# Optimization experiments

Hardware: AMD Instinct MI355X
Metric: run time of the kernel (lower is better)

The kernel has to match this reference:

```python
import jax, jax.numpy as jnp
import numpy as np

N = 50000   # nodes
E = 800000  # edges (avg degree 16)
DIMS = [(128, 128), (128, 128), (128, 64)]  # (in, out) per SAGEConv layer
EPS_BN = 1e-5
EPS_NORM = 1e-12


def _make_layer(key, din, dout):
    k1, k2 = jax.random.split(key)
    s = 1.0 / np.sqrt(din)
    return (
        jax.random.normal(k1, (dout, din), jnp.float32) * s,  # Wl: neighbor linear
        jnp.zeros((dout,), jnp.float32),                      # bl
        jax.random.normal(k2, (dout, din), jnp.float32) * s,  # Wr: root linear (no bias in PyG)
        jnp.ones((dout,), jnp.float32),                       # bn gamma
        jnp.zeros((dout,), jnp.float32),                      # bn beta
        jnp.zeros((dout,), jnp.float32),                      # bn running mean
        jnp.ones((dout,), jnp.float32),                       # bn running var
    )


def setup_inputs() -> dict:
    key = jax.random.key(0)
    kx, ke, k0, k1, k2 = jax.random.split(key, 5)
    inp = {
        "x": jax.random.normal(kx, (N, 128), jnp.float32),
        "edge_index": jax.random.randint(ke, (2, E), 0, N, dtype=jnp.int32),
    }
    for i, (k, (din, dout)) in enumerate(zip([k0, k1, k2], DIMS)):
        Wl, bl, Wr, g, b, rm, rv = _make_layer(k, din, dout)
        inp.update({f"Wl{i}": Wl, f"bl{i}": bl, f"Wr{i}": Wr,
                    f"g{i}": g, f"b{i}": b, f"rm{i}": rm, f"rv{i}": rv})
    return inp


def _sage_conv(x, src, dst, Wl, bl, Wr):
    # mean aggregation of incoming messages: gather src features, scatter-add at dst
    agg = jax.ops.segment_sum(x[src], dst, num_segments=N)          # [N, din]
    deg = jax.ops.segment_sum(jnp.ones((src.shape[0],), x.dtype), dst, num_segments=N)
    mean = agg / jnp.maximum(deg, 1.0)[:, None]
    return mean @ Wl.T + bl + x @ Wr.T


def _bn_eval(x, g, b, rm, rv):
    return g * (x - rm) * jax.lax.rsqrt(rv + EPS_BN) + b


def reference(x, edge_index,
              Wl0, bl0, Wr0, g0, b0, rm0, rv0,
              Wl1, bl1, Wr1, g1, b1, rm1, rv1,
              Wl2, bl2, Wr2, g2, b2, rm2, rv2):
    src, dst = edge_index[0], edge_index[1]
    layers = [
        (Wl0, bl0, Wr0, g0, b0, rm0, rv0),
        (Wl1, bl1, Wr1, g1, b1, rm1, rv1),
        (Wl2, bl2, Wr2, g2, b2, rm2, rv2),
    ]
    h = x
    for i, (Wl, bl, Wr, g, b, rm, rv) in enumerate(layers):
        h = _bn_eval(_sage_conv(h, src, dst, Wl, bl, Wr), g, b, rm, rv)
        if i < len(layers) - 1:
            h = jax.nn.relu(h)  # dropout is identity in eval mode
    # F.normalize(p=2, dim=1)
    return h / jnp.maximum(jnp.linalg.norm(h, axis=1, keepdims=True), EPS_NORM)
```

## Files before the change

### kernel.cpp

```cpp
#include <hip/hip_runtime.h>
#include <hip/hip_bf16.h>

#define CDIV(a,b) (((a)+(b)-1)/(b))
#define NBUCK_MAX 512
#define FUSE_CAP 4096
#define AGGF_CAP 3072

typedef __attribute__((ext_vector_type(8))) short short8;
typedef __attribute__((ext_vector_type(4))) float f32x4;
typedef __attribute__((ext_vector_type(2))) float f32x2;

static __device__ __forceinline__ unsigned short f2bf(float f){
  union { float f; unsigned u; } v; v.f = f;
  unsigned r = v.u + 0x7fffu + ((v.u >> 16) & 1u);
  return (unsigned short)(r >> 16);
}
static __device__ __forceinline__ unsigned pack2(float lo, float hi){
  return (unsigned)f2bf(lo) | ((unsigned)f2bf(hi) << 16);
}
static __device__ __forceinline__ float bf2f(unsigned short s){
  union { unsigned u; float f; } v; v.u = ((unsigned)s) << 16; return v.f;
}
static __device__ __forceinline__ unsigned pk_fp8x4(float a, float b, float c, float d){
  int v = __builtin_amdgcn_cvt_pk_fp8_f32(a, b, 0, false);
  v = __builtin_amdgcn_cvt_pk_fp8_f32(c, d, v, true);
  return (unsigned)v;
}

#define ACCP16(v) { b0 += __builtin_amdgcn_cvt_pk_f32_fp8((int)v.x, false); \
                    b1 += __builtin_amdgcn_cvt_pk_f32_fp8((int)v.x, true);  \
                    b2 += __builtin_amdgcn_cvt_pk_f32_fp8((int)v.y, false); \
                    b3 += __builtin_amdgcn_cvt_pk_f32_fp8((int)v.y, true);  \
                    b4 += __builtin_amdgcn_cvt_pk_f32_fp8((int)v.z, false); \
                    b5 += __builtin_amdgcn_cvt_pk_f32_fp8((int)v.z, true);  \
                    b6 += __builtin_amdgcn_cvt_pk_f32_fp8((int)v.w, false); \
                    b7 += __builtin_amdgcn_cvt_pk_f32_fp8((int)v.w, true); }


struct WtpArgs {
  const float *W0, *W1, *bl, *g, *b, *rm, *rv;
  unsigned short* Bpk; float *sc; float *sh;
  int kblk, dout, do_bn, nblk, perm;
};

static __device__ __forceinline__ void wtp_one(const WtpArgs& a, int idx){
  int NB16 = a.kblk*32*a.dout;
  if (idx < NB16){
    int j = idx & 7, lane = (idx >> 3) & 63, rest = idx >> 9;
    int NT = a.dout >> 4;
    int nt = rest % NT, kk = rest / NT;
    int nn = nt*16 + (lane & 15);
    int k  = kk*32 + ((lane >> 4) * 8) + j;
    float v;
    if (k < 128){
      int kc = a.perm ? (((k & 7) << 4) | (k >> 3)) : k;
      v = a.W0[nn*128 + kc];
    } else {
      v = a.W1[nn*128 + (k - 128)];
    }
    a.Bpk[idx] = f2bf(v);
  } else if (a.do_bn && idx < NB16 + a.dout){
    int jj = idx - NB16;
    float s = a.g[jj] * rsqrtf(a.rv[jj] + 1e-5f);
    a.sc[jj] = s;
    a.sh[jj] = (a.bl[jj] - a.rm[jj]) * s + a.b[jj];
  }
}


__global__ __launch_bounds__(256) void k_prep(const float* __restrict__ x, int n4, unsigned* __restrict__ xb,
                                              unsigned* __restrict__ xq,
                                              const int* __restrict__ dst, int E,
                                              int* __restrict__ bcnt, int nbuck,
                                              int castBlocks, int histBlocks,
                                              WtpArgs a0, WtpArgs a1, WtpArgs a2, WtpArgs a3){
  __shared__ int s[NBUCK_MAX];
  int b = blockIdx.x, t = threadIdx.x;
  if (b < castBlocks){
    int i = b*256 + t;
    if (i < n4){
      float4 v = ((const float4*)x)[i];
      uint2 o; o.x = pack2(v.x, v.y); o.y = pack2(v.z, v.w);
      ((uint2*)xb)[i] = o;
      xq[i] = pk_fp8x4(v.x, v.y, v.z, v.w);
    }
    return;
  }
  b -= castBlocks;
  if (b < histBlocks){
    for (int i=t;i<nbuck;i+=256) s[i] = 0;
    __syncthreads();
    constexpr int EPT = 16;
    int e0 = b*256*EPT;
    #pragma unroll
    for (int i=0;i<EPT;i++){
      int e = e0 + i*256 + t;
      if (e < E) atomicAdd(&s[dst[e] >> 7], 1);
    }
    __syncthreads();
    for (int i=t;i<nbuck;i+=256){
      int c = s[i];
      if (c > 0) atomicAdd(&bcnt[i], c);
    }
    return;
  }
  b -= histBlocks;
  if (b < a0.nblk){ wtp_one(a0, b*256 + t); return; }
  b -= a0.nblk;
  if (b < a1.nblk){ wtp_one(a1, b*256 + t); return; }
  b -= a1.nblk;
  if (b < a2.nblk){ wtp_one(a2, b*256 + t); return; }
  b -= a2.nblk;
  wtp_one(a3, b*256 + t);
}

__global__ __launch_bounds__(256) void k_bucketA(const int* __restrict__ src, const int* __restrict__ dst,
                                                 int E, const int* __restrict__ bcnt,
                                                 int* __restrict__ bcur, unsigned* __restrict__ ebuf, int nbuck){
  __shared__ int scnt[NBUCK_MAX];
  __shared__ int sbase[NBUCK_MAX];
  __shared__ int sboff[NBUCK_MAX];
  __shared__ int ss[256];
  int t = threadIdx.x;
  {
    int a0 = (2*t   < nbuck) ? bcnt[2*t]   : 0;
    int a1 = (2*t+1 < nbuck) ? bcnt[2*t+1] : 0;
    ss[t] = a0 + a1; __syncthreads();
    for (int d=1; d<256; d<<=1){
      int u = (t>=d) ? ss[t-d] : 0;
      __syncthreads();
      ss[t] += u;
      __syncthreads();
    }
    int excl = ss[t] - (a0 + a1);
    if (2*t   < nbuck) sboff[2*t]   = excl;
    if (2*t+1 < nbuck) sboff[2*t+1] = excl + a0;
  }
  for (int i=t;i<nbuck;i+=256) scnt[i] = 0;
  __syncthreads();
  constexpr int EPT = 16;
  int e0 = blockIdx.x*256*EPT;
  int b[EPT]; unsigned pk[EPT];
  #pragma unroll
  for (int i=0;i<EPT;i++){
    int e = e0 + i*256 + t;
    if (e < E){
      int d = dst[e];
      b[i] = d >> 7;
      pk[i] = ((unsigned)(d & 127) << 16) | (unsigned)src[e];
      atomicAdd(&scnt[b[i]], 1);
    } else b[i] = -1;
  }
  __syncthreads();
  for (int i=t;i<nbuck;i+=256){
    int c = scnt[i];
    sbase[i] = (c > 0) ? atomicAdd(&bcur[i], c) : 0;
    scnt[i] = 0;
  }
  __syncthreads();
  #pragma unroll
  for (int i=0;i<EPT;i++){
    if (b[i] >= 0){
      int p = atomicAdd(&scnt[b[i]], 1);
      ebuf[(size_t)sboff[b[i]] + sbase[b[i]] + p] = pk[i];
    }
  }
}

__global__ __launch_bounds__(256) void k_bucketB(const unsigned* __restrict__ ebuf, const int* __restrict__ bcnt,
                                                 int nbuck, int E, int N,
                                                 int* __restrict__ offR, int* __restrict__ csr,
                                                 int* __restrict__ nodemap){
  __shared__ int sEx[NBUCK_MAX];
  __shared__ int ss[256];
  __shared__ int sdeg[128];
  __shared__ int sabs[129];
  __shared__ int cur[128];
  __shared__ unsigned skey[128];
  __shared__ int rof[128];
  int b = blockIdx.x, t = threadIdx.x;
  {
    int a0 = (2*t   < nbuck) ? bcnt[2*t]   : 0;
    int a1 = (2*t+1 < nbuck) ? bcnt[2*t+1] : 0;
    ss[t] = a0 + a1; __syncthreads();
    for (int d=1; d<256; d<<=1){
      int u = (t>=d) ? ss[t-d] : 0;
      __syncthreads();
      ss[t] += u;
      __syncthreads();
    }
    int excl = ss[t] - (a0 + a1);
    if (2*t   < nbuck) sEx[2*t]   = excl;
    if (2*t+1 < nbuck) sEx[2*t+1] = excl + a0;
  }
  if (t < 128){ sdeg[t] = 0; cur[t] = 0; }
  __syncthreads();
  int e0 = sEx[b];
  int e1 = (b+1 < nbuck) ? sEx[b+1] : E;
  for (int e = e0 + t; e < e1; e += 256)
    atomicAdd(&sdeg[ebuf[e] >> 16], 1);
  __syncthreads();
  if (t < 128) skey[t] = ((unsigned)sdeg[t] << 7) | (unsigned)(127 - t);
  __syncthreads();
  #pragma unroll
  for (int k=2; k<=128; k<<=1){
    #pragma unroll
    for (int j=k>>1; j>0; j>>=1){
      if (t < 128){
        int p = t ^ j;
        if (p > t){
          unsigned x = skey[t], y = skey[p];
          bool swap = ((t & k) == 0) ? (x < y) : (x > y);
          if (swap){ skey[t] = y; skey[p] = x; }
        }
      }
      __syncthreads();
    }
  }
  if (t < 128){
    int lid = 127 - (int)(skey[t] & 127u);
    rof[lid] = t;
    sdeg[t] = (int)(skey[t] >> 7);
  }
  __syncthreads();
  for (int d=1; d<128; d<<=1){
    int u = (t < 128 && t >= d) ? sdeg[t-d] : 0;
    __syncthreads();
    if (t < 128) sdeg[t] += u;
    __syncthreads();
  }
  if (t == 0) sabs[0] = e0;
  if (t < 128) sabs[t+1] = e0 + sdeg[t];
  __syncthreads();
  int n0 = b << 7, n1 = min(n0 + 128, N);
  int cnt = n1 - n0;
  if (t <= cnt) offR[n0 + t] = sabs[t];
  if (t < cnt)  nodemap[n0 + t] = n0 + (127 - (int)(skey[t] & 127u));
  for (int e = e0 + t; e < e1; e += 256){
    unsigned pr = ebuf[e];
    int ln = (int)(pr >> 16);
    int p = atomicAdd(&cur[ln], 1);
    csr[sabs[rof[ln]] + p] = (int)(pr & 0xffffu);
  }
}


template<bool YL>
__global__ __launch_bounds__(256, 2) void k_fuse(
    const uint4* __restrict__ hq4, const int* __restrict__ offR, const int* __restrict__ csr,
    const int* __restrict__ nodemap,
    const unsigned short* __restrict__ Ag, const unsigned short* __restrict__ Bpk,
    const float* __restrict__ sc, const float* __restrict__ sh,
    const unsigned short* __restrict__ BpkL,
    unsigned short* __restrict__ outh, unsigned* __restrict__ outq,
    unsigned* __restrict__ outyl, int n){
  __shared__ uint4 Ms4[128*17];
  __shared__ uint4 sBL4[1024];
  __shared__ int sw[2];
  unsigned short* Ms = (unsigned short*)Ms4;
  int* scsr = (int*)sBL4;
  int t = threadIdx.x;
  int mb = blockIdx.x*128;
  if (t < 2) sw[t] = offR[min(mb + t*128, n)];
  __syncthreads();
  int e0b = sw[0];
  int span = sw[1] - e0b;
  for (int i = t; i < span && i < FUSE_CAP; i += 256) scsr[i] = csr[e0b + i];
  __syncthreads();

  int lane = t & 63, w = t >> 6;
  int sl = lane & 7;

  #pragma unroll
  for (int it=0; it<4; it++){
    int rk = w*32 + it*8 + (lane >> 3);
    int idx = mb + rk;
    bool valid = idx < n;
    int s0 = valid ? offR[idx]   : 0;
    int s1 = valid ? offR[idx+1] : 0;
    int ln = valid ? (nodemap[idx] - mb) : rk;
    f32x2 b0={0,0},b1={0,0},b2={0,0},b3={0,0},b4={0,0},b5={0,0},b6={0,0},b7={0,0};
    int e = s0;
    for (; e + 8 <= s1; e += 8){
      int le = e - e0b;
      int i0,i1,i2,i3,i4,i5,i6,i7;
      if (le + 8 <= FUSE_CAP){
        i0 = scsr[le];   i1 = scsr[le+1]; i2 = scsr[le+2]; i3 = scsr[le+3];
        i4 = scsr[le+4]; i5 = scsr[le+5]; i6 = scsr[le+6]; i7 = scsr[le+7];
      } else {
        i0 = csr[e];   i1 = csr[e+1]; i2 = csr[e+2]; i3 = csr[e+3];
        i4 = csr[e+4]; i5 = csr[e+5]; i6 = csr[e+6]; i7 = csr[e+7];
      }
      uint4 v0 = hq4[(size_t)i0*8 + sl];
      uint4 v1 = hq4[(size_t)i1*8 + sl];
      uint4 v2 = hq4[(size_t)i2*8 + sl];
      uint4 v3 = hq4[(size_t)i3*8 + sl];
      uint4 v4 = hq4[(size_t)i4*8 + sl];
      uint4 v5 = hq4[(size_t)i5*8 + sl];
      uint4 v6 = hq4[(size_t)i6*8 + sl];
      uint4 v7 = hq4[(size_t)i7*8 + sl];
      ACCP16(v0); ACCP16(v1); ACCP16(v2); ACCP16(v3);
      ACCP16(v4); ACCP16(v5); ACCP16(v6); ACCP16(v7);
    }
    for (; e + 4 <= s1; e += 4){
      int le = e - e0b;
      int i0,i1,i2,i3;
      if (le + 4 <= FUSE_CAP){
        i0 = scsr[le]; i1 = scsr[le+1]; i2 = scsr[le+2]; i3 = scsr[le+3];
      } else {
        i0 = csr[e]; i1 = csr[e+1]; i2 = csr[e+2]; i3 = csr[e+3];
      }
      uint4 v0 = hq4[(size_t)i0*8 + sl];
      uint4 v1 = hq4[(size_t)i1*8 + sl];
      uint4 v2 = hq4[(size_t)i2*8 + sl];
      uint4 v3 = hq4[(size_t)i3*8 + sl];
      ACCP16(v0); ACCP16(v1); ACCP16(v2); ACCP16(v3);
    }
    for (; e < s1; e++){
      int le = e - e0b;
      int ii = (le < FUSE_CAP) ? scsr[le] : csr[e];
      uint4 v = hq4[(size_t)ii*8 + sl];
      ACCP16(v);
    }
    int d = s1 - s0;
    float inv = 1.0f / (float)(d > 0 ? d : 1);
    uint4 o0, o1;
    o0.x = pack2(b0.x*inv, b0.y*inv);  o0.y = pack2(b1.x*inv, b1.y*inv);
    o0.z = pack2(b2.x*inv, b2.y*inv);  o0.w = pack2(b3.x*inv, b3.y*inv);
    o1.x = pack2(b4.x*inv, b4.y*inv);  o1.y = pack2(b5.x*inv, b5.y*inv);
    o1.z = pack2(b6.x*inv, b6.y*inv);  o1.w = pack2(b7.x*inv, b7.y*inv);
    Ms4[ln*17 + sl*2]     = o0;
    Ms4[ln*17 + sl*2 + 1] = o1;
  }
  __syncthreads();

  int quad = lane >> 4, c = lane & 15;
  int woff = w*32;
  int r0 = mb + woff + c;
  int r1 = r0 + 16;

  f32x4 acc[2][8];
  #pragma unroll
  for (int mt=0;mt<2;mt++)
    #pragma unroll
    for (int nt=0;nt<8;nt++) acc[mt][nt] = (f32x4){0.f,0.f,0.f,0.f};

  #pragma unroll
  for (int kk=0; kk<8; kk++){
    int ka = (kk & 3)*32 + quad*8;
    short8 a0, a1;
    if (kk < 4){
      a0 = *(const short8*)&Ms[(woff + c)*136 + ka];
      a1 = *(const short8*)&Ms[(woff + c + 16)*136 + ka];
    } else {
      a0 = (short8){0,0,0,0,0,0,0,0}; a1 = (short8){0,0,0,0,0,0,0,0};
      if (r0 < n) a0 = *(const short8*)(Ag + (size_t)r0*128 + ka);
      if (r1 < n) a1 = *(const short8*)(Ag + (size_t)r1*128 + ka);
    }
    #pragma unroll
    for (int nt=0; nt<8; nt++){
      short8 b = *(const short8*)(Bpk + (size_t)((kk*8 + nt)*64 + lane)*8);
      acc[0][nt] = __builtin_amdgcn_mfma_f32_16x16x32_bf16(a0, b, acc[0][nt], 0, 0, 0);
      acc[1][nt] = __builtin_amdgcn_mfma_f32_16x16x32_bf16(a1, b, acc[1][nt], 0, 0, 0);
    }
  }

  float scv[8], shv[8];
  #pragma unroll
  for (int nt=0;nt<8;nt++){ scv[nt] = sc[nt*16 + c]; shv[nt] = sh[nt*16 + c]; }

  if constexpr (YL) __syncthreads();

  #pragma unroll
  for (int mt=0; mt<2; mt++){
    #pragma unroll
    for (int r=0;r<4;r++){
      int lrow = woff + mt*16 + quad*4 + r;
      int row = mb + lrow;
      if (row < n){
        float u[8];
        #pragma unroll
        for (int nt=0;nt<8;nt++){
          float uu = acc[mt][nt][r]*scv[nt] + shv[nt];
          u[nt] = fmaxf(uu, 0.f);
          outh[(size_t)row*128 + nt*16 + c] = f2bf(u[nt]);
        }
        if constexpr (!YL){
          uint2 q;
          q.x = pk_fp8x4(u[0], u[1], u[2], u[3]);
          q.y = pk_fp8x4(u[4], u[5], u[6], u[7]);
          ((uint2*)outq)[(size_t)row*16 + c] = q;
        } else {
          #pragma unroll
          for (int nt=0;nt<8;nt++) Ms[lrow*136 + nt*16 + c] = f2bf(u[nt]);
        }
      } else if constexpr (YL) {
        #pragma unroll
        for (int nt=0;nt<8;nt++) Ms[lrow*136 + nt*16 + c] = 0;
      }
    }
  }

  if constexpr (YL){
    {
      const uint4* sL = (const uint4*)BpkL;
      #pragma unroll
      for (int i=0;i<4;i++) sBL4[i*256 + t] = sL[i*256 + t];
    }
    __syncthreads();
    unsigned short* BsL = (unsigned short*)sBL4;
    f32x4 acc2[2][4];
    #pragma unroll
    for (int mt=0;mt<2;mt++)
      #pragma unroll
      for (int nt=0;nt<4;nt++) acc2[mt][nt] = (f32x4){0.f,0.f,0.f,0.f};
    int r0l = woff + c, r1l = r0l + 16;
    #pragma unroll
    for (int kk=0; kk<4; kk++){
      int ka = kk*32 + quad*8;
      short8 a0 = *(const short8*)&Ms[r0l*136 + ka];
      short8 a1 = *(const short8*)&Ms[r1l*136 + ka];
      #pragma unroll
      for (int nt=0; nt<4; nt++){
        short8 b = *(const short8*)&BsL[(size_t)((kk*4 + nt)*64 + lane)*8];
        acc2[0][nt] = __builtin_amdgcn_mfma_f32_16x16x32_bf16(a0, b, acc2[0][nt], 0, 0, 0);
        acc2[1][nt] = __builtin_amdgcn_mfma_f32_16x16x32_bf16(a1, b, acc2[1][nt], 0, 0, 0);
      }
    }
    #pragma unroll
    for (int mt=0; mt<2; mt++){
      #pragma unroll
      for (int r=0;r<4;r++){
        int row = mb + woff + mt*16 + quad*4 + r;
        if (row < n){
          unsigned q  = pk_fp8x4(acc2[0][0][r], acc2[0][1][r], acc2[0][2][r], acc2[0][3][r]);
          unsigned q1 = pk_fp8x4(acc2[1][0][r], acc2[1][1][r], acc2[1][2][r], acc2[1][3][r]);
          outyl[(size_t)row*16 + c] = (mt == 0) ? q : q1;
        }
      }
    }
  }
}


__global__ __launch_bounds__(256, 2) void k_aggf(
    const uint4* __restrict__ ylq4, const int* __restrict__ offR, const int* __restrict__ csr,
    const int* __restrict__ nodemap,
    const unsigned short* __restrict__ A0, const unsigned short* __restrict__ BpkR,
    const float* __restrict__ sc, const float* __restrict__ sh,
    float* __restrict__ outf, int n){
  __shared__ unsigned short Ms[128*64];
  __shared__ unsigned short Bs[128*64];
  __shared__ int scsr[AGGF_CAP];
  __shared__ int sw[2];
  int t = threadIdx.x;
  int mb = blockIdx.x*128;
  if (t < 2) sw[t] = offR[min(mb + t*128, n)];
  {
    const uint4* s = (const uint4*)BpkR;
    uint4* d = (uint4*)Bs;
    #pragma unroll
    for (int i=0;i<4;i++) d[i*256 + t] = s[i*256 + t];
  }
  __syncthreads();
  int e0b = sw[0];
  int span = sw[1] - e0b;
  for (int i = t; i < span && i < AGGF_CAP; i += 256) scsr[i] = csr[e0b + i];
  __syncthreads();

  int lane = t & 63, w = t >> 6;
  int sl4 = lane & 3;

  #pragma unroll
  for (int it=0; it<2; it++){
    int rk = w*32 + it*16 + (lane >> 2);
    int idx = mb + rk;
    bool valid = idx < n;
    int s0 = valid ? offR[idx]   : 0;
    int s1 = valid ? offR[idx+1] : 0;
    int ln = valid ? (nodemap[idx] - mb) : rk;
    f32x2 b0={0,0},b1={0,0},b2={0,0},b3={0,0},b4={0,0},b5={0,0},b6={0,0},b7={0,0};
    int e = s0;
    for (; e + 8 <= s1; e += 8){
      int le = e - e0b;
      int i0,i1,i2,i3,i4,i5,i6,i7;
      if (le + 8 <= AGGF_CAP){
        i0 = scsr[le];   i1 = scsr[le+1]; i2 = scsr[le+2]; i3 = scsr[le+3];
        i4 = scsr[le+4]; i5 = scsr[le+5]; i6 = scsr[le+6]; i7 = scsr[le+7];
      } else {
        i0 = csr[e];   i1 = csr[e+1]; i2 = csr[e+2]; i3 = csr[e+3];
        i4 = csr[e+4]; i5 = csr[e+5]; i6 = csr[e+6]; i7 = csr[e+7];
      }
      uint4 v0 = ylq4[(size_t)i0*4 + sl4];
      uint4 v1 = ylq4[(size_t)i1*4 + sl4];
      uint4 v2 = ylq4[(size_t)i2*4 + sl4];
      uint4 v3 = ylq4[(size_t)i3*4 + sl4];
      uint4 v4 = ylq4[(size_t)i4*4 + sl4];
      uint4 v5 = ylq4[(size_t)i5*4 + sl4];
      uint4 v6 = ylq4[(size_t)i6*4 + sl4];
      uint4 v7 = ylq4[(size_t)i7*4 + sl4];
      ACCP16(v0); ACCP16(v1); ACCP16(v2); ACCP16(v3);
      ACCP16(v4); ACCP16(v5); ACCP16(v6); ACCP16(v7);
    }
    for (; e + 4 <= s1; e += 4){
      int le = e - e0b;
      int i0,i1,i2,i3;
      if (le + 4 <= AGGF_CAP){
        i0 = scsr[le]; i1 = scsr[le+1]; i2 = scsr[le+2]; i3 = scsr[le+3];
      } else {
        i0 = csr[e]; i1 = csr[e+1]; i2 = csr[e+2]; i3 = csr[e+3];
      }
      uint4 v0 = ylq4[(size_t)i0*4 + sl4];
      uint4 v1 = ylq4[(size_t)i1*4 + sl4];
      uint4 v2 = ylq4[(size_t)i2*4 + sl4];
      uint4 v3 = ylq4[(size_t)i3*4 + sl4];
      ACCP16(v0); ACCP16(v1); ACCP16(v2); ACCP16(v3);
    }
    for (; e < s1; e++){
      int le = e - e0b;
      int ii = (le < AGGF_CAP) ? scsr[le] : csr[e];
      uint4 v = ylq4[(size_t)ii*4 + sl4];
      ACCP16(v);
    }
    int d = s1 - s0;
    float inv = 1.0f / (float)(d > 0 ? d : 1);
    uint4 o0, o1;
    o0.x = pack2(b0.x*inv, b0.y*inv);  o0.y = pack2(b1.x*inv, b1.y*inv);
    o0.z = pack2(b2.x*inv, b2.y*inv);  o0.w = pack2(b3.x*inv, b3.y*inv);
    o1.x = pack2(b4.x*inv, b4.y*inv);  o1.y = pack2(b5.x*inv, b5.y*inv);
    o1.z = pack2(b6.x*inv, b6.y*inv);  o1.w = pack2(b7.x*inv, b7.y*inv);
    ((uint4*)Ms)[ln*8 + sl4*2]     = o0;
    ((uint4*)Ms)[ln*8 + sl4*2 + 1] = o1;
  }
  __syncthreads();

  int quad = lane >> 4, c = lane & 15;
  int woff = w*32;
  int r0 = mb + woff + c;
  int r1 = r0 + 16;
  f32x4 acc[2][4];
  #pragma unroll
  for (int mt=0;mt<2;mt++)
    #pragma unroll
    for (int nt=0;nt<4;nt++) acc[mt][nt] = (f32x4){0.f,0.f,0.f,0.f};
  #pragma unroll
  for (int kk=0; kk<4; kk++){
    int ka = kk*32 + quad*8;
    short8 a0 = {0,0,0,0,0,0,0,0}, a1 = {0,0,0,0,0,0,0,0};
    if (r0 < n) a0 = *(const short8*)(A0 + (size_t)r0*128 + ka);
    if (r1 < n) a1 = *(const short8*)(A0 + (size_t)r1*128 + ka);
    #pragma unroll
    for (int nt=0; nt<4; nt++){
      short8 b = *(const short8*)&Bs[(size_t)((kk*4 + nt)*64 + lane)*8];
      acc[0][nt] = __builtin_amdgcn_mfma_f32_16x16x32_bf16(a0, b, acc[0][nt], 0, 0, 0);
      acc[1][nt] = __builtin_amdgcn_mfma_f32_16x16x32_bf16(a1, b, acc[1][nt], 0, 0, 0);
    }
  }

  float scv[4], shv[4];
  #pragma unroll
  for (int nt=0;nt<4;nt++){ scv[nt] = sc[nt*16 + c]; shv[nt] = sh[nt*16 + c]; }

  #pragma unroll
  for (int mt=0; mt<2; mt++){
    #pragma unroll
    for (int r=0;r<4;r++){
      int lr = woff + mt*16 + quad*4 + r;
      int row = mb + lr;
      float v[4];
      float ss = 0.f;
      if (row < n){
        #pragma unroll
        for (int nt=0;nt<4;nt++){
          float u = acc[mt][nt][r] + bf2f(Ms[lr*64 + c*4 + nt]);
          u = u*scv[nt] + shv[nt];
          v[nt] = u;
          ss += u*u;
        }
      } else {
        #pragma unroll
        for (int nt=0;nt<4;nt++) v[nt] = 0.f;
      }
      ss += __shfl_xor(ss, 1, 64);
      ss += __shfl_xor(ss, 2, 64);
      ss += __shfl_xor(ss, 4, 64);
      ss += __shfl_xor(ss, 8, 64);
      float rn = 1.0f / fmaxf(sqrtf(ss), 1e-12f);
      if (row < n){
        #pragma unroll
        for (int nt=0;nt<4;nt++) outf[(size_t)row*64 + nt*16 + c] = v[nt]*rn;
      }
    }
  }
}


extern "C" void kernel_launch(void* const* d_in, const int* in_sizes, int n_in,
                              void* d_out, int out_size, void* d_ws, size_t ws_size,
                              hipStream_t stream){
  const float* x = (const float*)d_in[0];
  const int* ei  = (const int*)d_in[1];
  int N = in_sizes[0] / 128;
  int E = in_sizes[1] / 2;
  const int* esrc = ei;
  const int* edst = ei + E;
  int nbuck = CDIV(N, 128);

  const float *Wl[3], *bl[3], *Wr[3], *g[3], *bb[3], *rm[3], *rv[3];
  int dout[3];
  for (int i=0;i<3;i++){
    int base = 2 + 7*i;
    Wl[i]=(const float*)d_in[base];   bl[i]=(const float*)d_in[base+1];
    Wr[i]=(const float*)d_in[base+2]; g[i] =(const float*)d_in[base+3];
    bb[i]=(const float*)d_in[base+4]; rm[i]=(const float*)d_in[base+5];
    rv[i]=(const float*)d_in[base+6];
    dout[i] = in_sizes[base] / 128;
  }

  char* p = (char*)d_ws;
  size_t o = 0;
  auto alloc = [&](size_t bytes)->void*{ void* r = p + o; o += (bytes + 255) & ~(size_t)255; return r; };
  int* bz    = (int*)alloc((size_t)2*nbuck*4);
  int* bcnt  = bz;
  int* bcur  = bz + nbuck;
  int* offR  = (int*)alloc((size_t)(N+1)*4);
  int* nodemap = (int*)alloc((size_t)N*4);
  int* csr   = (int*)alloc((size_t)E*4);
  unsigned* ebuf = (unsigned*)alloc((size_t)E*4);
  unsigned* xb   = (unsigned*)alloc((size_t)N*64*4);
  unsigned* xq   = (unsigned*)alloc((size_t)N*128);
  unsigned* h_a  = (unsigned*)alloc((size_t)N*64*4);
  unsigned* haq  = (unsigned*)alloc((size_t)N*128);
  unsigned* h_b  = (unsigned*)alloc((size_t)N*64*4);
  unsigned* ylb  = (unsigned*)alloc((size_t)N*64);
  unsigned short* Bpk01[2];
  float* sc[3]; float* sh[3];
  for (int i=0;i<2;i++) Bpk01[i] = (unsigned short*)alloc((size_t)256*dout[i]*2);
  unsigned short* BpkL = (unsigned short*)alloc((size_t)128*dout[2]*2);
  unsigned short* BpkR = (unsigned short*)alloc((size_t)128*dout[2]*2);
  for (int i=0;i<3;i++){
    sc[i] = (float*)alloc((size_t)dout[i]*4);
    sh[i] = (float*)alloc((size_t)dout[i]*4);
  }

  hipMemsetAsync(bz, 0, (size_t)2*nbuck*4, stream);

  WtpArgs wa[4];
  wa[0] = { Wl[0], Wr[0], bl[0], g[0], bb[0], rm[0], rv[0], Bpk01[0], sc[0], sh[0], 8, dout[0], 1, CDIV(256*dout[0]+dout[0],256), 0 };
  wa[1] = { Wl[1], Wr[1], bl[1], g[1], bb[1], rm[1], rv[1], Bpk01[1], sc[1], sh[1], 8, dout[1], 1, CDIV(256*dout[1]+dout[1],256), 1 };
  wa[2] = { Wl[2], nullptr, nullptr, nullptr, nullptr, nullptr, nullptr, BpkL, nullptr, nullptr, 4, dout[2], 0, CDIV(128*dout[2],256), 0 };
  wa[3] = { Wr[2], nullptr, bl[2], g[2], bb[2], rm[2], rv[2], BpkR, sc[2], sh[2], 4, dout[2], 1, CDIV(128*dout[2]+dout[2],256), 0 };

  int castBlocks = CDIV(N*32, 256);
  int histBlocks = CDIV(E, 256*16);
  int prepBlocks = castBlocks + histBlocks + wa[0].nblk + wa[1].nblk + wa[2].nblk + wa[3].nblk;
  k_prep   <<<prepBlocks,256,0,stream>>>(x, N*32, xb, xq, edst, E, bcnt, nbuck, castBlocks, histBlocks,
                                         wa[0], wa[1], wa[2], wa[3]);
  k_bucketA<<<CDIV(E,256*16),256,0,stream>>>(esrc, edst, E, bcnt, bcur, ebuf, nbuck);
  k_bucketB<<<nbuck,256,0,stream>>>(ebuf, bcnt, nbuck, E, N, offR, csr, nodemap);

  k_fuse<false><<<nbuck,256,0,stream>>>((const uint4*)xq, offR, csr, nodemap,
                                        (const unsigned short*)xb, Bpk01[0], sc[0], sh[0], nullptr,
                                        (unsigned short*)h_a, haq, nullptr, N);
  k_fuse<true><<<nbuck,256,0,stream>>>((const uint4*)haq, offR, csr, nodemap,
                                       (const unsigned short*)h_a, Bpk01[1], sc[1], sh[1], BpkL,
                                       (unsigned short*)h_b, nullptr, ylb, N);
  k_aggf<<<nbuck,256,0,stream>>>((const uint4*)ylb, offR, csr, nodemap,
                                 (const unsigned short*)h_b, BpkR, sc[2], sh[2],
                                 (float*)d_out, N);
}
```

Baseline: 242.8 us.

## Fuse CSR bucket build into first SAGE layer and drop degree-sorted node remap

Merges the second bucketing pass (per-bucket CSR construction) with the first layer's gather-aggregate-GEMM kernel, building the bucket's CSR slice directly in shared memory and reusing it for aggregation. The bitonic sort of nodes by degree and the nodemap indirection are removed, so rows are processed in natural order. Launch bounds are raised to allow three blocks per CU. This removes one kernel launch, a global CSR round-trip, and the sort barriers, at the cost of losing degree-based load balancing within waves and extra shared memory in the fused kernel.

```diff
diff --git a/kernel.cpp b/kernel.cpp
--- a/kernel.cpp
+++ b/kernel.cpp
@@ -3,8 +3,7 @@
 
 #define CDIV(a,b) (((a)+(b)-1)/(b))
 #define NBUCK_MAX 512
-#define FUSE_CAP 4096
-#define AGGF_CAP 3072
+#define FUSE_CAP 3072
 
 typedef __attribute__((ext_vector_type(8))) short short8;
 typedef __attribute__((ext_vector_type(4))) float f32x4;
@@ -167,17 +166,21 @@
   }
 }
 
-__global__ __launch_bounds__(256) void k_bucketB(const unsigned* __restrict__ ebuf, const int* __restrict__ bcnt,
-                                                 int nbuck, int E, int N,
-                                                 int* __restrict__ offR, int* __restrict__ csr,
-                                                 int* __restrict__ nodemap){
+
+__global__ __launch_bounds__(256, 3) void k_bfuse(
+    const unsigned* __restrict__ ebuf, const int* __restrict__ bcnt, int nbuck, int E, int N,
+    int* __restrict__ off, int* __restrict__ csr,
+    const uint4* __restrict__ xq4, const unsigned short* __restrict__ Ag,
+    const unsigned short* __restrict__ Bpk, const float* __restrict__ sc, const float* __restrict__ sh,
+    unsigned short* __restrict__ outh, unsigned* __restrict__ outq){
+  __shared__ uint4 Ms4[128*17];
+  __shared__ int scsr[FUSE_CAP];
   __shared__ int sEx[NBUCK_MAX];
   __shared__ int ss[256];
-  __shared__ int sdeg[128];
-  __shared__ int sabs[129];
-  __shared__ int cur[128];
-  __shared__ unsigned skey[128];
-  __shared__ int rof[128];
+  unsigned short* Ms = (unsigned short*)Ms4;
+  int* sdeg = (int*)Ms4;
+  int* sabs = sdeg + 128;
+  int* cur  = sabs + 129;
   int b = blockIdx.x, t = threadIdx.x;
   {
     int a0 = (2*t   < nbuck) ? bcnt[2*t]   : 0;
@@ -197,31 +200,10 @@
   __syncthreads();
   int e0 = sEx[b];
   int e1 = (b+1 < nbuck) ? sEx[b+1] : E;
+  int span = e1 - e0;
+  bool fits = span <= FUSE_CAP;
   for (int e = e0 + t; e < e1; e += 256)
     atomicAdd(&sdeg[ebuf[e] >> 16], 1);
-  __syncthreads();
-  if (t < 128) skey[t] = ((unsigned)sdeg[t] << 7) | (unsigned)(127 - t);
-  __syncthreads();
-  #pragma unroll
-  for (int k=2; k<=128; k<<=1){
-    #pragma unroll
-    for (int j=k>>1; j>0; j>>=1){
-      if (t < 128){
-        int p = t ^ j;
-        if (p > t){
-          unsigned x = skey[t], y = skey[p];
-          bool swap = ((t & k) == 0) ? (x < y) : (x > y);
-          if (swap){ skey[t] = y; skey[p] = x; }
-        }
-      }
-      __syncthreads();
-    }
-  }
-  if (t < 128){
-    int lid = 127 - (int)(skey[t] & 127u);
-    rof[lid] = t;
-    sdeg[t] = (int)(skey[t] >> 7);
-  }
   __syncthreads();
   for (int d=1; d<128; d<<=1){
     int u = (t < 128 && t >= d) ? sdeg[t-d] : 0;
@@ -229,31 +211,157 @@
     if (t < 128) sdeg[t] += u;
     __syncthreads();
   }
-  if (t == 0) sabs[0] = e0;
-  if (t < 128) sabs[t+1] = e0 + sdeg[t];
+  if (t == 0) sabs[0] = 0;
+  if (t < 128) sabs[t+1] = sdeg[t];
   __syncthreads();
   int n0 = b << 7, n1 = min(n0 + 128, N);
   int cnt = n1 - n0;
-  if (t <= cnt) offR[n0 + t] = sabs[t];
-  if (t < cnt)  nodemap[n0 + t] = n0 + (127 - (int)(skey[t] & 127u));
+  if (t <= cnt) off[n0 + t] = e0 + sabs[t];
+  int lane = t & 63, w = t >> 6, sl = lane & 7;
+  int gs0[4], gs1[4];
+  #pragma unroll
+  for (int it=0; it<4; it++){
+    int rk = w*32 + it*8 + (lane >> 3);
+    gs0[it] = sabs[rk];
+    gs1[it] = sabs[rk+1];
+  }
   for (int e = e0 + t; e < e1; e += 256){
     unsigned pr = ebuf[e];
     int ln = (int)(pr >> 16);
     int p = atomicAdd(&cur[ln], 1);
-    csr[sabs[rof[ln]] + p] = (int)(pr & 0xffffu);
-  }
-}
-
-
-template<bool YL>
-__global__ __launch_bounds__(256, 2) void k_fuse(
-    const uint4* __restrict__ hq4, const int* __restrict__ offR, const int* __restrict__ csr,
-    const int* __restrict__ nodemap,
+    int loc = sabs[ln] + p;
+    int sv = (int)(pr & 0xffffu);
+    if (fits) scsr[loc] = sv;
+    else      csr[e0 + loc] = sv;
+  }
+  __syncthreads();
+  if (fits){
+    for (int i = t; i < span; i += 256) csr[e0 + i] = scsr[i];
+  } else {
+    for (int i = t; i < FUSE_CAP; i += 256) scsr[i] = csr[e0 + i];
+    __syncthreads();
+  }
+
+  #pragma unroll
+  for (int it=0; it<4; it++){
+    int rk = w*32 + it*8 + (lane >> 3);
+    int s0 = gs0[it], s1 = gs1[it];
+    f32x2 b0={0,0},b1={0,0},b2={0,0},b3={0,0},b4={0,0},b5={0,0},b6={0,0},b7={0,0};
+    int e = s0;
+    for (; e + 8 <= s1; e += 8){
+      int i0,i1,i2,i3,i4,i5,i6,i7;
+      if (e + 8 <= FUSE_CAP){
+        i0 = scsr[e];   i1 = scsr[e+1]; i2 = scsr[e+2]; i3 = scsr[e+3];
+        i4 = scsr[e+4]; i5 = scsr[e+5]; i6 = scsr[e+6]; i7 = scsr[e+7];
+      } else {
+        i0 = csr[e0+e];   i1 = csr[e0+e+1]; i2 = csr[e0+e+2]; i3 = csr[e0+e+3];
+        i4 = csr[e0+e+4]; i5 = csr[e0+e+5]; i6 = csr[e0+e+6]; i7 = csr[e0+e+7];
+      }
+      uint4 v0 = xq4[(size_t)i0*8 + sl];
+      uint4 v1 = xq4[(size_t)i1*8 + sl];
+      uint4 v2 = xq4[(size_t)i2*8 + sl];
+      uint4 v3 = xq4[(size_t)i3*8 + sl];
+      uint4 v4 = xq4[(size_t)i4*8 + sl];
+      uint4 v5 = xq4[(size_t)i5*8 + sl];
+      uint4 v6 = xq4[(size_t)i6*8 + sl];
+      uint4 v7 = xq4[(size_t)i7*8 + sl];
+      ACCP16(v0); ACCP16(v1); ACCP16(v2); ACCP16(v3);
+      ACCP16(v4); ACCP16(v5); ACCP16(v6); ACCP16(v7);
+    }
+    for (; e + 4 <= s1; e += 4){
+      int i0,i1,i2,i3;
+      if (e + 4 <= FUSE_CAP){
+        i0 = scsr[e]; i1 = scsr[e+1]; i2 = scsr[e+2]; i3 = scsr[e+3];
+      } else {
+        i0 = csr[e0+e]; i1 = csr[e0+e+1]; i2 = csr[e0+e+2]; i3 = csr[e0+e+3];
+      }
+      uint4 v0 = xq4[(size_t)i0*8 + sl];
+      uint4 v1 = xq4[(size_t)i1*8 + sl];
+      uint4 v2 = xq4[(size_t)i2*8 + sl];
+      uint4 v3 = xq4[(size_t)i3*8 + sl];
+      ACCP16(v0); ACCP16(v1); ACCP16(v2); ACCP16(v3);
+    }
+    for (; e < s1; e++){
+      int ii = (e < FUSE_CAP) ? scsr[e] : csr[e0+e];
+      uint4 v = xq4[(size_t)ii*8 + sl];
+      ACCP16(v);
+    }
+    int d = s1 - s0;
+    float inv = 1.0f / (float)(d > 0 ? d : 1);
+    uint4 o0, o1;
+    o0.x = pack2(b0.x*inv, b0.y*inv);  o0.y = pack2(b1.x*inv, b1.y*inv);
+    o0.z = pack2(b2.x*inv, b2.y*inv);  o0.w = pack2(b3.x*inv, b3.y*inv);
+    o1.x = pack2(b4.x*inv, b4.y*inv);  o1.y = pack2(b5.x*inv, b5.y*inv);
+    o1.z = pack2(b6.x*inv, b6.y*inv);  o1.w = pack2(b7.x*inv, b7.y*inv);
+    Ms4[rk*17 + sl*2]     = o0;
+    Ms4[rk*17 + sl*2 + 1] = o1;
+  }
+  __syncthreads();
+
+  int quad = lane >> 4, c = lane & 15;
+  int mb = n0, woff = w*32;
+  int r0 = mb + woff + c;
+  int r1 = r0 + 16;
+
+  f32x4 acc[2][8];
+  #pragma unroll
+  for (int mt=0;mt<2;mt++)
+    #pragma unroll
+    for (int nt=0;nt<8;nt++) acc[mt][nt] = (f32x4){0.f,0.f,0.f,0.f};
+
+  #pragma unroll
+  for (int kk=0; kk<8; kk++){
+    int ka = (kk & 3)*32 + quad*8;
+    short8 a0, a1;
+    if (kk < 4){
+      a0 = *(const short8*)&Ms[(woff + c)*136 + ka];
+      a1 = *(const short8*)&Ms[(woff + c + 16)*136 + ka];
+    } else {
+      a0 = (short8){0,0,0,0,0,0,0,0}; a1 = (short8){0,0,0,0,0,0,0,0};
+      if (r0 < N) a0 = *(const short8*)(Ag + (size_t)r0*128 + ka);
+      if (r1 < N) a1 = *(const short8*)(Ag + (size_t)r1*128 + ka);
+    }
+    #pragma unroll
+    for (int nt=0; nt<8; nt++){
+      short8 bb = *(const short8*)(Bpk + (size_t)((kk*8 + nt)*64 + lane)*8);
+      acc[0][nt] = __builtin_amdgcn_mfma_f32_16x16x32_bf16(a0, bb, acc[0][nt], 0, 0, 0);
+      acc[1][nt] = __builtin_amdgcn_mfma_f32_16x16x32_bf16(a1, bb, acc[1][nt], 0, 0, 0);
+    }
+  }
+
+  float scv[8], shv[8];
+  #pragma unroll
+  for (int nt=0;nt<8;nt++){ scv[nt] = sc[nt*16 + c]; shv[nt] = sh[nt*16 + c]; }
+
+  #pragma unroll
+  for (int mt=0; mt<2; mt++){
+    #pragma unroll
+    for (int r=0;r<4;r++){
+      int row = mb + woff + mt*16 + quad*4 + r;
+      if (row < N){
+        float u[8];
+        #pragma unroll
+        for (int nt=0;nt<8;nt++){
+          float uu = acc[mt][nt][r]*scv[nt] + shv[nt];
+          u[nt] = fmaxf(uu, 0.f);
+          outh[(size_t)row*128 + nt*16 + c] = f2bf(u[nt]);
+        }
+        uint2 q;
+        q.x = pk_fp8x4(u[0], u[1], u[2], u[3]);
+        q.y = pk_fp8x4(u[4], u[5], u[6], u[7]);
+        ((uint2*)outq)[(size_t)row*16 + c] = q;
+      }
+    }
+  }
+}
+
+
+__global__ __launch_bounds__(256, 3) void k_fuse1(
+    const uint4* __restrict__ hq4, const int* __restrict__ off, const int* __restrict__ csr,
     const unsigned short* __restrict__ Ag, const unsigned short* __restrict__ Bpk,
     const float* __restrict__ sc, const float* __restrict__ sh,
     const unsigned short* __restrict__ BpkL,
-    unsigned short* __restrict__ outh, unsigned* __restrict__ outq,
-    unsigned* __restrict__ outyl, int n){
+    unsigned short* __restrict__ outh, unsigned* __restrict__ outyl, int n){
   __shared__ uint4 Ms4[128*17];
   __shared__ uint4 sBL4[1024];
   __shared__ int sw[2];
@@ -261,11 +369,12 @@
   int* scsr = (int*)sBL4;
   int t = threadIdx.x;
   int mb = blockIdx.x*128;
-  if (t < 2) sw[t] = offR[min(mb + t*128, n)];
+  if (t < 2) sw[t] = off[min(mb + t*128, n)];
   __syncthreads();
   int e0b = sw[0];
   int span = sw[1] - e0b;
-  for (int i = t; i < span && i < FUSE_CAP; i += 256) scsr[i] = csr[e0b + i];
+  int CAPL = 4096;
+  for (int i = t; i < span && i < CAPL; i += 256) scsr[i] = csr[e0b + i];
   __syncthreads();
 
   int lane = t & 63, w = t >> 6;
@@ -276,15 +385,14 @@
     int rk = w*32 + it*8 + (lane >> 3);
     int idx = mb + rk;
     bool valid = idx < n;
-    int s0 = valid ? offR[idx]   : 0;
-    int s1 = valid ? offR[idx+1] : 0;
-    int ln = valid ? (nodemap[idx] - mb) : rk;
+    int s0 = valid ? off[idx]   : 0;
+    int s1 = valid ? off[idx+1] : 0;
     f32x2 b0={0,0},b1={0,0},b2={0,0},b3={0,0},b4={0,0},b5={0,0},b6={0,0},b7={0,0};
     int e = s0;
     for (; e + 8 <= s1; e += 8){
       int le = e - e0b;
       int i0,i1,i2,i3,i4,i5,i6,i7;
-      if (le + 8 <= FUSE_CAP){
+      if (le + 8 <= CAPL){
         i0 = scsr[le];   i1 = scsr[le+1]; i2 = scsr[le+2]; i3 = scsr[le+3];
         i4 = scsr[le+4]; i5 = scsr[le+5]; i6 = scsr[le+6]; i7 = scsr[le+7];
       } else {
@@ -305,7 +413,7 @@
     for (; e + 4 <= s1; e += 4){
       int le = e - e0b;
       int i0,i1,i2,i3;
-      if (le + 4 <= FUSE_CAP){
+      if (le + 4 <= CAPL){
         i0 = scsr[le]; i1 = scsr[le+1]; i2 = scsr[le+2]; i3 = scsr[le+3];
       } else {
         i0 = csr[e]; i1 = csr[e+1]; i2 = csr[e+2]; i3 = csr[e+3];
@@ -318,7 +426,7 @@
     }
     for (; e < s1; e++){
       int le = e - e0b;
-      int ii = (le < FUSE_CAP) ? scsr[le] : csr[e];
+      int ii = (le < CAPL) ? scsr[le] : csr[e];
       uint4 v = hq4[(size_t)ii*8 + sl];
       ACCP16(v);
     }
@@ -329,8 +437,8 @@
     o0.z = pack2(b2.x*inv, b2.y*inv);  o0.w = pack2(b3.x*inv, b3.y*inv);
     o1.x = pack2(b4.x*inv, b4.y*inv);  o1.y = pack2(b5.x*inv, b5.y*inv);
     o1.z = pack2(b6.x*inv, b6.y*inv);  o1.w = pack2(b7.x*inv, b7.y*inv);
-    Ms4[ln*17 + sl*2]     = o0;
-    Ms4[ln*17 + sl*2 + 1] = o1;
+    Ms4[rk*17 + sl*2]     = o0;
+    Ms4[rk*17 + sl*2 + 1] = o1;
   }
   __syncthreads();
 
@@ -359,9 +467,9 @@
     }
     #pragma unroll
     for (int nt=0; nt<8; nt++){
-      short8 b = *(const short8*)(Bpk + (size_t)((kk*8 + nt)*64 + lane)*8);
-      acc[0][nt] = __builtin_amdgcn_mfma_f32_16x16x32_bf16(a0, b, acc[0][nt], 0, 0, 0);
-      acc[1][nt] = __builtin_amdgcn_mfma_f32_16x16x32_bf16(a1, b, acc[1][nt], 0, 0, 0);
+      short8 bb = *(const short8*)(Bpk + (size_t)((kk*8 + nt)*64 + lane)*8);
+      acc[0][nt] = __builtin_amdgcn_mfma_f32_16x16x32_bf16(a0, bb, acc[0][nt], 0, 0, 0);
+      acc[1][nt] = __builtin_amdgcn_mfma_f32_16x16x32_bf16(a1, bb, acc[1][nt], 0, 0, 0);
     }
   }
 
@@ -369,7 +477,7 @@
   #pragma unroll
   for (int nt=0;nt<8;nt++){ scv[nt] = sc[nt*16 + c]; shv[nt] = sh[nt*16 + c]; }
 
-  if constexpr (YL) __syncthreads();
+  __syncthreads();
 
   #pragma unroll
   for (int mt=0; mt<2; mt++){
@@ -385,67 +493,59 @@
           u[nt] = fmaxf(uu, 0.f);
           outh[(size_t)row*128 + nt*16 + c] = f2bf(u[nt]);
         }
-        if constexpr (!YL){
-          uint2 q;
-          q.x = pk_fp8x4(u[0], u[1], u[2], u[3]);
-          q.y = pk_fp8x4(u[4], u[5], u[6], u[7]);
-          ((uint2*)outq)[(size_t)row*16 + c] = q;
-        } else {
-          #pragma unroll
-          for (int nt=0;nt<8;nt++) Ms[lrow*136 + nt*16 + c] = f2bf(u[nt]);
-        }
-      } else if constexpr (YL) {
+        #pragma unroll
+        for (int nt=0;nt<8;nt++) Ms[lrow*136 + nt*16 + c] = f2bf(u[nt]);
+      } else {
         #pragma unroll
         for (int nt=0;nt<8;nt++) Ms[lrow*136 + nt*16 + c] = 0;
       }
     }
   }
 
-  if constexpr (YL){
-    {
-      const uint4* sL = (const uint4*)BpkL;
-      #pragma unroll
-      for (int i=0;i<4;i++) sBL4[i*256 + t] = sL[i*256 + t];
-    }
-    __syncthreads();
-    unsigned short* BsL = (unsigned short*)sBL4;
-    f32x4 acc2[2][4];
-    #pragma unroll
-    for (int mt=0;mt<2;mt++)
-      #pragma unroll
-      for (int nt=0;nt<4;nt++) acc2[mt][nt] = (f32x4){0.f,0.f,0.f,0.f};
-    int r0l = woff + c, r1l = r0l + 16;
-    #pragma unroll
-    for (int kk=0; kk<4; kk++){
-      int ka = kk*32 + quad*8;
-      short8 a0 = *(const short8*)&Ms[r0l*136 + ka];
-      short8 a1 = *(const short8*)&Ms[r1l*136 + ka];
-      #pragma unroll
-      for (int nt=0; nt<4; nt++){
-        short8 b = *(const short8*)&BsL[(size_t)((kk*4 + nt)*64 + lane)*8];
-        acc2[0][nt] = __builtin_amdgcn_mfma_f32_16x16x32_bf16(a0, b, acc2[0][nt], 0, 0, 0);
-        acc2[1][nt] = __builtin_amdgcn_mfma_f32_16x16x32_bf16(a1, b, acc2[1][nt], 0, 0, 0);
-      }
-    }
-    #pragma unroll
-    for (int mt=0; mt<2; mt++){
-      #pragma unroll
-      for (int r=0;r<4;r++){
-        int row = mb + woff + mt*16 + quad*4 + r;
-        if (row < n){
-          unsigned q  = pk_fp8x4(acc2[0][0][r], acc2[0][1][r], acc2[0][2][r], acc2[0][3][r]);
-          unsigned q1 = pk_fp8x4(acc2[1][0][r], acc2[1][1][r], acc2[1][2][r], acc2[1][3][r]);
-          outyl[(size_t)row*16 + c] = (mt == 0) ? q : q1;
-        }
-      }
-    }
-  }
-}
-
-
-__global__ __launch_bounds__(256, 2) void k_aggf(
-    const uint4* __restrict__ ylq4, const int* __restrict__ offR, const int* __restrict__ csr,
-    const int* __restrict__ nodemap,
+  {
+    const uint4* sL = (const uint4*)BpkL;
+    #pragma unroll
+    for (int i=0;i<4;i++) sBL4[i*256 + t] = sL[i*256 + t];
+  }
+  __syncthreads();
+  unsigned short* BsL = (unsigned short*)sBL4;
+  f32x4 acc2[2][4];
+  #pragma unroll
+  for (int mt=0;mt<2;mt++)
+    #pragma unroll
+    for (int nt=0;nt<4;nt++) acc2[mt][nt] = (f32x4){0.f,0.f,0.f,0.f};
+  int r0l = woff + c, r1l = r0l + 16;
+  #pragma unroll
+  for (int kk=0; kk<4; kk++){
+    int ka = kk*32 + quad*8;
+    short8 a0 = *(const short8*)&Ms[r0l*136 + ka];
+    short8 a1 = *(const short8*)&Ms[r1l*136 + ka];
+    #pragma unroll
+    for (int nt=0; nt<4; nt++){
+      short8 bb = *(const short8*)&BsL[(size_t)((kk*4 + nt)*64 + lane)*8];
+      acc2[0][nt] = __builtin_amdgcn_mfma_f32_16x16x32_bf16(a0, bb, acc2[0][nt], 0, 0, 0);
+      acc2[1][nt] = __builtin_amdgcn_mfma_f32_16x16x32_bf16(a1, bb, acc2[1][nt], 0, 0, 0);
+    }
+  }
+  #pragma unroll
+  for (int mt=0; mt<2; mt++){
+    #pragma unroll
+    for (int r=0;r<4;r++){
+      int row = mb + woff + mt*16 + quad*4 + r;
+      if (row < n){
+        unsigned q  = pk_fp8x4(acc2[0][0][r], acc2[0][1][r], acc2[0][2][r], acc2[0][3][r]);
+        unsigned q1 = pk_fp8x4(acc2[1][0][r], acc2[1][1][r], acc2[1][2][r], acc2[1][3][r]);
+        outyl[(size_t)row*16 + c] = (mt == 0) ? q : q1;
+      }
+    }
+  }
+}
+
+
+#define AGGF_CAP 3072
+
+__global__ __launch_bounds__(256, 3) void k_aggf(
+    const uint4* __restrict__ ylq4, const int* __restrict__ off, const int* __restrict__ csr,
     const unsigned short* __restrict__ A0, const unsigned short* __restrict__ BpkR,
     const float* __restrict__ sc, const float* __restrict__ sh,
     float* __restrict__ outf, int n){
@@ -455,7 +555,7 @@
   __shared__ int sw[2];
   int t = threadIdx.x;
   int mb = blockIdx.x*128;
-  if (t < 2) sw[t] = offR[min(mb + t*128, n)];
+  if (t < 2) sw[t] = off[min(mb + t*128, n)];
   {
     const uint4* s = (const uint4*)BpkR;
     uint4* d = (uint4*)Bs;
@@ -476,9 +576,8 @@
     int rk = w*32 + it*16 + (lane >> 2);
     int idx = mb + rk;
     bool valid = idx < n;
-    int s0 = valid ? offR[idx]   : 0;
-    int s1 = valid ? offR[idx+1] : 0;
-    int ln = valid ? (nodemap[idx] - mb) : rk;
+    int s0 = valid ? off[idx]   : 0;
+    int s1 = valid ? off[idx+1] : 0;
     f32x2 b0={0,0},b1={0,0},b2={0,0},b3={0,0},b4={0,0},b5={0,0},b6={0,0},b7={0,0};
     int e = s0;
     for (; e + 8 <= s1; e += 8){
@@ -529,8 +628,8 @@
     o0.z = pack2(b2.x*inv, b2.y*inv);  o0.w = pack2(b3.x*inv, b3.y*inv);
     o1.x = pack2(b4.x*inv, b4.y*inv);  o1.y = pack2(b5.x*inv, b5.y*inv);
     o1.z = pack2(b6.x*inv, b6.y*inv);  o1.w = pack2(b7.x*inv, b7.y*inv);
-    ((uint4*)Ms)[ln*8 + sl4*2]     = o0;
-    ((uint4*)Ms)[ln*8 + sl4*2 + 1] = o1;
+    ((uint4*)Ms)[rk*8 + sl4*2]     = o0;
+    ((uint4*)Ms)[rk*8 + sl4*2 + 1] = o1;
   }
   __syncthreads();
 
@@ -551,9 +650,9 @@
     if (r1 < n) a1 = *(const short8*)(A0 + (size_t)r1*128 + ka);
     #pragma unroll
     for (int nt=0; nt<4; nt++){
-      short8 b = *(const short8*)&Bs[(size_t)((kk*4 + nt)*64 + lane)*8];
-      acc[0][nt] = __builtin_amdgcn_mfma_f32_16x16x32_bf16(a0, b, acc[0][nt], 0, 0, 0);
-      acc[1][nt] = __builtin_amdgcn_mfma_f32_16x16x32_bf16(a1, b, acc[1][nt], 0, 0, 0);
+      short8 bb = *(const short8*)&Bs[(size_t)((kk*4 + nt)*64 + lane)*8];
+      acc[0][nt] = __builtin_amdgcn_mfma_f32_16x16x32_bf16(a0, bb, acc[0][nt], 0, 0, 0);
+      acc[1][nt] = __builtin_amdgcn_mfma_f32_16x16x32_bf16(a1, bb, acc[1][nt], 0, 0, 0);
     }
   }
 
@@ -623,8 +722,7 @@
   int* bz    = (int*)alloc((size_t)2*nbuck*4);
   int* bcnt  = bz;
   int* bcur  = bz + nbuck;
-  int* offR  = (int*)alloc((size_t)(N+1)*4);
-  int* nodemap = (int*)alloc((size_t)N*4);
+  int* off   = (int*)alloc((size_t)(N+1)*4);
   int* csr   = (int*)alloc((size_t)E*4);
   unsigned* ebuf = (unsigned*)alloc((size_t)E*4);
   unsigned* xb   = (unsigned*)alloc((size_t)N*64*4);
@@ -657,15 +755,15 @@
   k_prep   <<<prepBlocks,256,0,stream>>>(x, N*32, xb, xq, edst, E, bcnt, nbuck, castBlocks, histBlocks,
                                          wa[0], wa[1], wa[2], wa[3]);
   k_bucketA<<<CDIV(E,256*16),256,0,stream>>>(esrc, edst, E, bcnt, bcur, ebuf, nbuck);
-  k_bucketB<<<nbuck,256,0,stream>>>(ebuf, bcnt, nbuck, E, N, offR, csr, nodemap);
-
-  k_fuse<false><<<nbuck,256,0,stream>>>((const uint4*)xq, offR, csr, nodemap,
-                                        (const unsigned short*)xb, Bpk01[0], sc[0], sh[0], nullptr,
-                                        (unsigned short*)h_a, haq, nullptr, N);
-  k_fuse<true><<<nbuck,256,0,stream>>>((const uint4*)haq, offR, csr, nodemap,
-                                       (const unsigned short*)h_a, Bpk01[1], sc[1], sh[1], BpkL,
-                                       (unsigned short*)h_b, nullptr, ylb, N);
-  k_aggf<<<nbuck,256,0,stream>>>((const uint4*)ylb, offR, csr, nodemap,
+
+  k_bfuse<<<nbuck,256,0,stream>>>(ebuf, bcnt, nbuck, E, N, off, csr,
+                                  (const uint4*)xq, (const unsigned short*)xb,
+                                  Bpk01[0], sc[0], sh[0],
+                                  (unsigned short*)h_a, haq);
+  k_fuse1<<<nbuck,256,0,stream>>>((const uint4*)haq, off, csr,
+                                  (const unsigned short*)h_a, Bpk01[1], sc[1], sh[1], BpkL,
+                                  (unsigned short*)h_b, ylb, N);
+  k_aggf<<<nbuck,256,0,stream>>>((const uint4*)ylb, off, csr,
                                  (const unsigned short*)h_b, BpkR, sc[2], sh[2],
                                  (float*)d_out, N);
 }
```

After: 236.1 us. 1.03x faster.
